# Kernel optimization log

Hardware: AMD Instinct MI355X
Metric: run time of the kernel (lower is better)

The kernel has to match this reference:

```python
import math
import jax, jax.numpy as jnp
import numpy as np

LN_EPS = 1e-5


def _layernorm(x, g, b):
    m = jnp.mean(x, axis=-1, keepdims=True)
    v = jnp.var(x, axis=-1, keepdims=True)
    return (x - m) / jnp.sqrt(v + LN_EPS) * g + b


def setup_inputs() -> dict:
    key = jax.random.key(0)
    ks = jax.random.split(key, 14)
    B, C, H, W = 8, 96, 224, 224
    dim, hidden = 96, int(96 * 4.0)

    def lin(k, i, o):
        return jax.random.normal(k, (i, o), jnp.float32) * 0.02

    return {
        "x": jax.random.normal(ks[0], (B, C, H, W), jnp.float32),
        "entropy_map": jax.random.uniform(ks[1], (B, 1, H, W), jnp.float32),
        "beta": jnp.float32(1.0),
        "wq": lin(ks[2], dim, dim), "bq": jnp.zeros((dim,), jnp.float32),
        "wk": lin(ks[3], dim, dim), "bk": jnp.zeros((dim,), jnp.float32),
        "wv": lin(ks[4], dim, dim), "bv": jnp.zeros((dim,), jnp.float32),
        "wo": lin(ks[5], dim, dim), "bo": jnp.zeros((dim,), jnp.float32),
        "ln1_g": jnp.ones((dim,), jnp.float32), "ln1_b": jnp.zeros((dim,), jnp.float32),
        "ln2_g": jnp.ones((dim,), jnp.float32), "ln2_b": jnp.zeros((dim,), jnp.float32),
        "w_fc1": lin(ks[6], dim, hidden), "b_fc1": jnp.zeros((hidden,), jnp.float32),
        "w_fc2": lin(ks[7], hidden, dim), "b_fc2": jnp.zeros((dim,), jnp.float32),
    }


def reference(x, entropy_map, beta, wq, bq, wk, bk, wv, bv, wo, bo,
              ln1_g, ln1_b, ln2_g, ln2_b, w_fc1, b_fc1, w_fc2, b_fc2):
    B, C, H, W = x.shape
    ws = 7
    num_heads = 4
    hd = C // num_heads
    nHw, nWw = H // ws, W // ws
    N = ws * ws

    # (B,C,H,W) -> (B,H,W,C), norm1
    xt = jnp.transpose(x, (0, 2, 3, 1))
    xn = _layernorm(xt, ln1_g, ln1_b)

    # window partition -> (B*nW, N, C)
    xw = xn.reshape(B, nHw, ws, nWw, ws, C).transpose(0, 1, 3, 2, 4, 5).reshape(-1, N, C)
    ew = entropy_map.transpose(0, 2, 3, 1).reshape(B, nHw, ws, nWw, ws, 1)
    ew = ew.transpose(0, 1, 3, 2, 4, 5).reshape(-1, N, 1)  # (Bw, N, 1)

    Bw = xw.shape[0]
    q = (jnp.einsum('bnc,cd->bnd', xw, wq) + bq).reshape(Bw, N, num_heads, hd).transpose(0, 2, 1, 3)
    k = (jnp.einsum('bnc,cd->bnd', xw, wk) + bk).reshape(Bw, N, num_heads, hd).transpose(0, 2, 1, 3)
    v = (jnp.einsum('bnc,cd->bnd', xw, wv) + bv).reshape(Bw, N, num_heads, hd).transpose(0, 2, 1, 3)

    scores = jnp.einsum('bhqd,bhkd->bhqk', q, k) / math.sqrt(hd)
    attn = jax.nn.softmax(scores, axis=-1)

    # entropy gating: per-query factor (Bw,1,N,1), then renormalize over keys
    gating = jnp.exp(-beta * ew)[:, None, :, :]
    attn = attn * gating
    attn = attn / (jnp.sum(attn, axis=-1, keepdims=True) + 1e-9)

    out = jnp.einsum('bhqk,bhkd->bhqd', attn, v).transpose(0, 2, 1, 3).reshape(Bw, N, C)
    out = jnp.einsum('bnc,cd->bnd', out, wo) + bo

    # window merge -> (B,H,W,C)
    out = out.reshape(B, nHw, nWw, ws, ws, C).transpose(0, 1, 3, 2, 4, 5).reshape(B, H, W, C)

    x_res = xt + out  # (B,H,W,C)

    # MLP branch
    xn2 = _layernorm(x_res, ln2_g, ln2_b)
    h = jax.nn.gelu(jnp.einsum('bhwc,cd->bhwd', xn2, w_fc1) + b_fc1, approximate=False)
    mlp_out = jnp.einsum('bhwd,dc->bhwc', h, w_fc2) + b_fc2

    x_out = x_res + mlp_out
    return jnp.transpose(x_out, (0, 3, 1, 2))  # (B,C,H,W)
```

## Files before the change

### kernel.cpp

```cpp
#include <hip/hip_runtime.h>
#include <math.h>

typedef __attribute__((ext_vector_type(8))) short short8;
typedef __attribute__((ext_vector_type(4))) float f32x4;
typedef __attribute__((ext_vector_type(4))) unsigned int uint4v;

struct __align__(8) U2 { unsigned int x, y; };

#define DEVI static __device__ __forceinline__

DEVI unsigned pk1(float f){ unsigned u = __float_as_uint(f); return (u + 0x7fffu + ((u>>16)&1u)) >> 16; }
DEVI unsigned pk2(float a, float b){ return pk1(a) | (pk1(b) << 16); }
DEVI float bfu(unsigned hs){ return __uint_as_float((hs & 0xffffu) << 16); }

DEVI short8 lds8(const unsigned short* p){
  union { short8 v; U2 u[2]; } f;
  f.u[0] = *(const U2*)p;
  f.u[1] = *(const U2*)(p + 4);
  return f.v;
}
DEVI short8 mk8(unsigned a, unsigned b, unsigned c, unsigned d){
  union { short8 v; unsigned u[4]; } f; f.u[0]=a; f.u[1]=b; f.u[2]=c; f.u[3]=d; return f.v;
}
DEVI short8 zero8(){ return mk8(0,0,0,0); }
DEVI short8 gfrag(const unsigned short* p){ union { short8 v; uint4v u; } f; f.u = *(const uint4v*)p; return f.v; }
DEVI f32x4 MFMA(short8 a, short8 b, f32x4 c){ return __builtin_amdgcn_mfma_f32_16x16x32_bf16(a, b, c, 0, 0, 0); }
DEVI void st2(unsigned short* p, unsigned lo, unsigned hi){ U2 t; t.x=lo; t.y=hi; *(U2*)p = t; }

DEVI float fastrcp(float x){ float r; asm("v_rcp_f32 %0, %1" : "=v"(r) : "v"(x)); return r; }
DEVI float gelu_f(float v){
  float z2 = fmaf(v*v*v, -0.07135481627f, -1.5957691216f*v);
  return v * fastrcp(1.f + __expf(z2));
}

__global__ __launch_bounds__(256) void prep_kernel(
    const float* __restrict__ wq, const float* __restrict__ wk,
    const float* __restrict__ wv, const float* __restrict__ wo,
    const float* __restrict__ w1, const float* __restrict__ w2,
    unsigned short* __restrict__ wfr)
{
  int i = blockIdx.x * 256 + threadIdx.x;
  if (i >= 110592) return;
  int j = i & 7, lane = (i >> 3) & 63, fr = i >> 9;
  int ln = lane & 15, lg = lane >> 4;
  float v;
  if (fr < 18)      { int s = fr;       int mt = s/3,  kb = s%3;  v = wq[(32*kb + 8*lg + j)*96  + 16*mt + ln]; }
  else if (fr < 36) { int s = fr - 18;  int mt = s/3,  kb = s%3;  v = wk[(32*kb + 8*lg + j)*96  + 16*mt + ln]; }
  else if (fr < 54) { int s = fr - 36;  int nt = s/3,  kb = s%3;  v = wv[(32*kb + 8*lg + j)*96  + 16*nt + ln]; }
  else if (fr < 72) { int s = fr - 54;  int mt = s/3,  kb = s%3;  v = wo[(32*kb + 8*lg + j)*96  + 16*mt + ln]; }
  else if (fr < 144){ int s = fr - 72;  int mt = s/3,  kb = s%3;  v = w1[(32*kb + 8*lg + j)*384 + 16*mt + ln]; }
  else              { int s = fr - 144; int mt = s/12, kb = s%12; v = w2[(32*kb + 8*lg + j)*96  + 16*mt + ln]; }
  wfr[i] = (unsigned short)pk1(v);
}

__global__ __launch_bounds__(256, 4) void attn_kernel(
    const float* __restrict__ x, const float* __restrict__ emap,
    const float* __restrict__ beta_p,
    const float* __restrict__ bq, const float* __restrict__ bk,
    const float* __restrict__ bv, const float* __restrict__ bo,
    const float* __restrict__ g1, const float* __restrict__ b1,
    const unsigned short* __restrict__ wfr,
    unsigned short* __restrict__ xres)
{
  __shared__ __align__(16) char smem[39744];
  unsigned short* XN = (unsigned short*)(smem);
  unsigned short* KS = (unsigned short*)(smem + 12800);
  unsigned short* VT = (unsigned short*)(smem + 25600);

  const int tid = threadIdx.x;
  const int lane = tid & 63;
  const int w = tid >> 6, lg = lane >> 4, ln = lane & 15;

  int bid = blockIdx.x;
  int bw  = ((bid & 7) << 10) | (bid >> 3);
  const int b  = bw >> 10;
  const int rr = bw & 1023;
  const int h0 = (rr >> 5) * 7;
  const int w0 = (rr & 31) * 7;

  for (int i = tid; i < 8*68; i += 256) VT[(96 + i/68)*68 + i%68] = 0;

  float ewv = 0.f;
  {
    const int t = 16*w + ln;
    float xv[24];
    if (t < 49){
      size_t pixloc = (size_t)(h0 + t/7)*224 + w0 + t%7;
      const float* xp = x + (size_t)(b*96 + 24*lg)*50176 + pixloc;
#pragma unroll
      for (int i = 0; i < 24; ++i) xv[i] = xp[(size_t)i*50176];
      ewv = emap[(size_t)b*50176 + pixloc];
    } else {
#pragma unroll
      for (int i = 0; i < 24; ++i) xv[i] = 0.f;
    }
    float s = 0.f, s2 = 0.f;
#pragma unroll
    for (int i = 0; i < 24; ++i){ s += xv[i]; s2 += xv[i]*xv[i]; }
    s  += __shfl_xor(s, 16);  s  += __shfl_xor(s, 32);
    s2 += __shfl_xor(s2, 16); s2 += __shfl_xor(s2, 32);
    float m = s * (1.f/96.f);
    float var = s2 * (1.f/96.f) - m*m;
    float rstd = rsqrtf(var + 1e-5f);
    unsigned* w32 = (unsigned*)(XN + t*100 + 24*lg);
    if (t < 49){
#pragma unroll
      for (int i = 0; i < 12; ++i){
        int c = 24*lg + 2*i;
        w32[i] = pk2((xv[2*i]   - m)*rstd*g1[c]   + b1[c],
                     (xv[2*i+1] - m)*rstd*g1[c+1] + b1[c+1]);
      }
    } else {
#pragma unroll
      for (int i = 0; i < 12; ++i) w32[i] = 0;
    }
  }
  __syncthreads();

  unsigned qp[6][2];
  {
    short8 bx0 = lds8(XN + (16*w+ln)*100 + 0  + 8*lg);
    short8 bx1 = lds8(XN + (16*w+ln)*100 + 32 + 8*lg);
    short8 bx2 = lds8(XN + (16*w+ln)*100 + 64 + 8*lg);
#pragma unroll
    for (int mt = 0; mt < 6; ++mt){
      int d0 = 16*mt + 4*lg;
      f32x4 aq, ak;
#pragma unroll
      for (int r = 0; r < 4; ++r){ aq[r] = bq[d0+r]; ak[r] = bk[d0+r]; }
      aq = MFMA(gfrag(wfr +        (mt*3+0)*512 + lane*8), bx0, aq);
      aq = MFMA(gfrag(wfr +        (mt*3+1)*512 + lane*8), bx1, aq);
      aq = MFMA(gfrag(wfr +        (mt*3+2)*512 + lane*8), bx2, aq);
      ak = MFMA(gfrag(wfr + 9216 + (mt*3+0)*512 + lane*8), bx0, ak);
      ak = MFMA(gfrag(wfr + 9216 + (mt*3+1)*512 + lane*8), bx1, ak);
      ak = MFMA(gfrag(wfr + 9216 + (mt*3+2)*512 + lane*8), bx2, ak);
      qp[mt][0] = pk2(aq[0],aq[1]);
      qp[mt][1] = pk2(aq[2],aq[3]);
      st2(KS + (16*w+ln)*100 + d0, pk2(ak[0],ak[1]), pk2(ak[2],ak[3]));
    }
#pragma unroll
    for (int f = 0; f < 6; ++f){
      int fl = f*4 + w;
      int mt = fl / 6, nt = fl % 6;
      float bvv = bv[16*nt + ln];
      f32x4 av; av[0]=bvv; av[1]=bvv; av[2]=bvv; av[3]=bvv;
#pragma unroll
      for (int kb = 0; kb < 3; ++kb)
        av = MFMA(lds8(XN + (16*mt+ln)*100 + 32*kb + 8*lg),
                  gfrag(wfr + 18432 + (nt*3+kb)*512 + lane*8), av);
      st2(VT + (16*nt+ln)*68 + 16*mt + 4*lg, pk2(av[0],av[1]), pk2(av[2],av[3]));
    }
  }
  __syncthreads();

  const float beta  = beta_p[0];
  const float scale = 0.20412414523193150818f;
  const float gq    = __expf(-beta * ewv);
  const int  psrcA  = ((lg & 1) << 5) + ln;
  const int  psrcB  = psrcA + 16;
  const bool phi    = (lg >= 2);

#pragma unroll
  for (int h = 0; h < 4; ++h){
    const int mlo = (6*h) >> 2, mhi = mlo + 1;
    const int thr = (h & 1) ? 1 : 2;
    int par  = (3*h + lg) & 1;
    int srcA = (par << 5) + ln;
    int srcB = srcA + 16;
    unsigned lA0 = __shfl(qp[mlo][0], srcA), lA1 = __shfl(qp[mlo][1], srcA);
    unsigned hA0 = __shfl(qp[mhi][0], srcA), hA1 = __shfl(qp[mhi][1], srcA);
    unsigned lB0 = __shfl(qp[mlo][0], srcB), lB1 = __shfl(qp[mlo][1], srcB);
    unsigned hB0 = __shfl(qp[mhi][0], srcB), hB1 = __shfl(qp[mhi][1], srcB);
    bool uh = (lg >= thr);
    short8 bqf = (lg < 3) ? mk8(uh?hA0:lA0, uh?hA1:lA1, uh?hB0:lB0, uh?hB1:lB1) : zero8();

    f32x4 sva[4];
#pragma unroll
    for (int mt = 0; mt < 4; ++mt){
      f32x4 z; z[0]=0.f; z[1]=0.f; z[2]=0.f; z[3]=0.f;
      short8 af = (lg < 3) ? lds8(KS + (16*mt+ln)*100 + 24*h + 8*lg) : zero8();
      sva[mt] = MFMA(af, bqf, z);
    }
    float vv[16]; float mx = -3e38f;
#pragma unroll
    for (int mt = 0; mt < 4; ++mt)
#pragma unroll
      for (int r = 0; r < 4; ++r){
        int key = 16*mt + 4*lg + r;
        float v = (key <= 48) ? sva[mt][r]*scale : -3e38f;
        vv[mt*4+r] = v; mx = fmaxf(mx, v);
      }
    mx = fmaxf(mx, __shfl_xor(mx, 16));
    mx = fmaxf(mx, __shfl_xor(mx, 32));
    float ssum = 0.f;
#pragma unroll
    for (int i = 0; i < 16; ++i){ float e = __expf(vv[i] - mx); vv[i] = e; ssum += e; }
    ssum += __shfl_xor(ssum, 16);
    ssum += __shfl_xor(ssum, 32);
    float inv = gq / (ssum * (gq + 1e-9f));

    unsigned pu[4][2];
#pragma unroll
    for (int mt = 0; mt < 4; ++mt){
      pu[mt][0] = pk2(vv[4*mt+0]*inv, vv[4*mt+1]*inv);
      pu[mt][1] = pk2(vv[4*mt+2]*inv, vv[4*mt+3]*inv);
    }
    unsigned a00=__shfl(pu[0][0],psrcA), a01=__shfl(pu[0][1],psrcA);
    unsigned a10=__shfl(pu[1][0],psrcA), a11=__shfl(pu[1][1],psrcA);
    unsigned b00=__shfl(pu[0][0],psrcB), b01=__shfl(pu[0][1],psrcB);
    unsigned b10=__shfl(pu[1][0],psrcB), b11=__shfl(pu[1][1],psrcB);
    short8 pf0 = mk8(phi?a10:a00, phi?a11:a01, phi?b10:b00, phi?b11:b01);
    unsigned c00=__shfl(pu[2][0],psrcA), c01=__shfl(pu[2][1],psrcA);
    unsigned c10=__shfl(pu[3][0],psrcA), c11=__shfl(pu[3][1],psrcA);
    unsigned d00=__shfl(pu[2][0],psrcB), d01=__shfl(pu[2][1],psrcB);
    unsigned d10=__shfl(pu[3][0],psrcB), d11=__shfl(pu[3][1],psrcB);
    short8 pf1 = mk8(phi?c10:c00, phi?c11:c01, phi?d10:d00, phi?d11:d01);

#pragma unroll
    for (int mt = 0; mt < 2; ++mt){
      f32x4 pv; pv[0]=0.f; pv[1]=0.f; pv[2]=0.f; pv[3]=0.f;
      pv = MFMA(lds8(VT + (24*h+16*mt+ln)*68 + 0  + 8*lg), pf0, pv);
      pv = MFMA(lds8(VT + (24*h+16*mt+ln)*68 + 32 + 8*lg), pf1, pv);
      if (!(mt == 1 && lg >= 2))
        st2(XN + (16*w+ln)*100 + 24*h + 16*mt + 4*lg, pk2(pv[0],pv[1]), pk2(pv[2],pv[3]));
    }
  }

  {
    f32x4 po[6];
#pragma unroll
    for (int mt = 0; mt < 6; ++mt){
      int c0 = 16*mt + 4*lg;
#pragma unroll
      for (int r = 0; r < 4; ++r) po[mt][r] = bo[c0+r];
    }
#pragma unroll
    for (int kb = 0; kb < 3; ++kb){
      short8 bf_ = lds8(XN + (16*w+ln)*100 + 32*kb + 8*lg);
#pragma unroll
      for (int mt = 0; mt < 6; ++mt)
        po[mt] = MFMA(gfrag(wfr + 27648 + (mt*3+kb)*512 + lane*8), bf_, po[mt]);
    }
    const int t = 16*w + ln;
    if (t < 49){
      size_t pixloc = (size_t)(h0 + t/7)*224 + w0 + t%7;
      const float* xp = x + (size_t)b*96*50176 + pixloc;
      unsigned short* xo = xres + ((size_t)b*50176 + pixloc)*96;
#pragma unroll
      for (int mt = 0; mt < 6; ++mt){
        int c0 = 16*mt + 4*lg;
        float r0 = po[mt][0] + xp[(size_t)(c0+0)*50176];
        float r1 = po[mt][1] + xp[(size_t)(c0+1)*50176];
        float r2 = po[mt][2] + xp[(size_t)(c0+2)*50176];
        float r3 = po[mt][3] + xp[(size_t)(c0+3)*50176];
        st2(xo + c0, pk2(r0,r1), pk2(r2,r3));
      }
    }
  }
}

__global__ __launch_bounds__(256, 4) void mlp_kernel(
    const unsigned short* __restrict__ xres,
    const float* __restrict__ g2, const float* __restrict__ b2,
    const float* __restrict__ bf1, const float* __restrict__ bf2,
    const unsigned short* __restrict__ wfr,
    float* __restrict__ out)
{
  __shared__ __align__(16) unsigned short XH[4][4800];
  const int tid = threadIdx.x, lane = tid & 63, w = tid >> 6;
  const int lg = lane >> 4, ln = lane & 15;
  unsigned short* XN2 = &XH[w][0];
  unsigned short* HS  = &XH[w][1600];

  const int tile = blockIdx.x*4 + w;
  const size_t p0 = (size_t)tile * 16;
  const int bimg = (int)(p0 / 50176);
  const size_t pixin = p0 - (size_t)bimg*50176;

  {
    const unsigned* xp = (const unsigned*)(xres + (p0 + (size_t)ln)*96 + 24*lg);
    float xv[24];
#pragma unroll
    for (int i = 0; i < 12; ++i){
      unsigned u = xp[i];
      xv[2*i] = bfu(u); xv[2*i+1] = bfu(u >> 16);
    }
    float s = 0.f, s2 = 0.f;
#pragma unroll
    for (int i = 0; i < 24; ++i){ s += xv[i]; s2 += xv[i]*xv[i]; }
    s  += __shfl_xor(s, 16);  s  += __shfl_xor(s, 32);
    s2 += __shfl_xor(s2, 16); s2 += __shfl_xor(s2, 32);
    float m = s * (1.f/96.f);
    float var = s2 * (1.f/96.f) - m*m;
    float rstd = rsqrtf(var + 1e-5f);
    unsigned* w32 = (unsigned*)(XN2 + ln*100 + 24*lg);
#pragma unroll
    for (int i = 0; i < 12; ++i){
      int c = 24*lg + 2*i;
      w32[i] = pk2((xv[2*i]   - m)*rstd*g2[c]   + b2[c],
                   (xv[2*i+1] - m)*rstd*g2[c+1] + b2[c+1]);
    }
  }

  f32x4 oacc[6];
#pragma unroll
  for (int mt = 0; mt < 6; ++mt){
    int c0 = 16*mt + 4*lg;
#pragma unroll
    for (int r = 0; r < 4; ++r) oacc[mt][r] = bf2[c0+r];
  }

  short8 bxx0 = lds8(XN2 + ln*100 + 0  + 8*lg);
  short8 bxx1 = lds8(XN2 + ln*100 + 32 + 8*lg);
  short8 bxx2 = lds8(XN2 + ln*100 + 64 + 8*lg);

#pragma unroll
  for (int p = 0; p < 2; ++p){
#pragma unroll
    for (int mt = 0; mt < 12; ++mt){
      int hg = p*192 + 16*mt + 4*lg;
      f32x4 ha;
#pragma unroll
      for (int r = 0; r < 4; ++r) ha[r] = bf1[hg+r];
      ha = MFMA(gfrag(wfr + 36864 + ((p*12+mt)*3+0)*512 + lane*8), bxx0, ha);
      ha = MFMA(gfrag(wfr + 36864 + ((p*12+mt)*3+1)*512 + lane*8), bxx1, ha);
      ha = MFMA(gfrag(wfr + 36864 + ((p*12+mt)*3+2)*512 + lane*8), bxx2, ha);
      st2(HS + ln*200 + 16*mt + 4*lg,
          pk2(gelu_f(ha[0]), gelu_f(ha[1])), pk2(gelu_f(ha[2]), gelu_f(ha[3])));
    }
#pragma unroll
    for (int kb = 0; kb < 6; ++kb){
      short8 bh = lds8(HS + ln*200 + 32*kb + 8*lg);
#pragma unroll
      for (int mt = 0; mt < 6; ++mt)
        oacc[mt] = MFMA(gfrag(wfr + 73728 + (mt*12 + p*6 + kb)*512 + lane*8), bh, oacc[mt]);
    }
  }

  {
    const unsigned short* xr = xres + (p0 + (size_t)ln)*96;
    float* ob = out + (size_t)bimg*96*50176 + pixin + ln;
#pragma unroll
    for (int mt = 0; mt < 6; ++mt){
      int c0 = 16*mt + 4*lg;
      U2 rv = *(const U2*)(xr + c0);
      ob[(size_t)(c0+0)*50176] = oacc[mt][0] + bfu(rv.x);
      ob[(size_t)(c0+1)*50176] = oacc[mt][1] + bfu(rv.x >> 16);
      ob[(size_t)(c0+2)*50176] = oacc[mt][2] + bfu(rv.y);
      ob[(size_t)(c0+3)*50176] = oacc[mt][3] + bfu(rv.y >> 16);
    }
  }
}

extern "C" void kernel_launch(void* const* d_in, const int* in_sizes, int n_in,
                              void* d_out, int out_size, void* d_ws, size_t ws_size,
                              hipStream_t stream) {
  const float* x    = (const float*)d_in[0];
  const float* emap = (const float*)d_in[1];
  const float* beta = (const float*)d_in[2];
  const float* wq   = (const float*)d_in[3];
  const float* bq   = (const float*)d_in[4];
  const float* wk   = (const float*)d_in[5];
  const float* bk   = (const float*)d_in[6];
  const float* wv   = (const float*)d_in[7];
  const float* bv   = (const float*)d_in[8];
  const float* wo   = (const float*)d_in[9];
  const float* bo   = (const float*)d_in[10];
  const float* g1   = (const float*)d_in[11];
  const float* b1   = (const float*)d_in[12];
  const float* g2   = (const float*)d_in[13];
  const float* b2   = (const float*)d_in[14];
  const float* w1   = (const float*)d_in[15];
  const float* bf1  = (const float*)d_in[16];
  const float* w2   = (const float*)d_in[17];
  const float* bf2  = (const float*)d_in[18];

  float* out = (float*)d_out;
  unsigned short* wfr  = (unsigned short*)d_ws;
  unsigned short* xres = (unsigned short*)((char*)d_ws + 262144);

  prep_kernel<<<dim3(432), dim3(256), 0, stream>>>(wq, wk, wv, wo, w1, w2, wfr);
  attn_kernel<<<dim3(8192), dim3(256), 0, stream>>>(
      x, emap, beta, bq, bk, bv, bo, g1, b1, wfr, xres);
  mlp_kernel<<<dim3(6272), dim3(256), 0, stream>>>(
      xres, g2, b2, bf1, bf2, wfr, out);
}
```

Before: 429.9 us.

## Fold attention scale into Wq, drop softmax max, reuse loaded x for residuals

Pre-scales Wq and bq by 1/sqrt(hd) so scores need no extra multiply. The softmax max-reduction is replaced by a fixed -50 bias on padded keys, and normalization moves to the P·V output via a fast reciprocal. Q is now staged through LDS instead of register shuffles. The x values loaded for LayerNorm are kept in registers and reused for the residual add in both kernels, removing a second global read of x and of xres. This uses more LDS and registers, so occupancy drops from 4 to 3 blocks. Dropping the max subtraction assumes scores stay small enough for exp not to overflow.

```diff
diff --git a/kernel.cpp b/kernel.cpp
--- a/kernel.cpp
+++ b/kernel.cpp
@@ -44,7 +44,7 @@
   int j = i & 7, lane = (i >> 3) & 63, fr = i >> 9;
   int ln = lane & 15, lg = lane >> 4;
   float v;
-  if (fr < 18)      { int s = fr;       int mt = s/3,  kb = s%3;  v = wq[(32*kb + 8*lg + j)*96  + 16*mt + ln]; }
+  if (fr < 18)      { int s = fr;       int mt = s/3,  kb = s%3;  v = wq[(32*kb + 8*lg + j)*96  + 16*mt + ln] * 0.20412414523193150818f; }
   else if (fr < 36) { int s = fr - 18;  int mt = s/3,  kb = s%3;  v = wk[(32*kb + 8*lg + j)*96  + 16*mt + ln]; }
   else if (fr < 54) { int s = fr - 36;  int nt = s/3,  kb = s%3;  v = wv[(32*kb + 8*lg + j)*96  + 16*nt + ln]; }
   else if (fr < 72) { int s = fr - 54;  int mt = s/3,  kb = s%3;  v = wo[(32*kb + 8*lg + j)*96  + 16*mt + ln]; }
@@ -53,7 +53,7 @@
   wfr[i] = (unsigned short)pk1(v);
 }
 
-__global__ __launch_bounds__(256, 4) void attn_kernel(
+__global__ __launch_bounds__(256, 3) void attn_kernel(
     const float* __restrict__ x, const float* __restrict__ emap,
     const float* __restrict__ beta_p,
     const float* __restrict__ bq, const float* __restrict__ bk,
@@ -62,10 +62,11 @@
     const unsigned short* __restrict__ wfr,
     unsigned short* __restrict__ xres)
 {
-  __shared__ __align__(16) char smem[39744];
+  __shared__ __align__(16) char smem[52544];
   unsigned short* XN = (unsigned short*)(smem);
-  unsigned short* KS = (unsigned short*)(smem + 12800);
-  unsigned short* VT = (unsigned short*)(smem + 25600);
+  unsigned short* QS = (unsigned short*)(smem + 12800);
+  unsigned short* KS = (unsigned short*)(smem + 25600);
+  unsigned short* VT = (unsigned short*)(smem + 38400);
 
   const int tid = threadIdx.x;
   const int lane = tid & 63;
@@ -78,17 +79,18 @@
   const int h0 = (rr >> 5) * 7;
   const int w0 = (rr & 31) * 7;
 
-  for (int i = tid; i < 8*68; i += 256) VT[(96 + i/68)*68 + i%68] = 0;
-
+  const int t = 16*w + ln;
+
+  float xv[24];
   float ewv = 0.f;
   {
-    const int t = 16*w + ln;
-    float xv[24];
     if (t < 49){
       size_t pixloc = (size_t)(h0 + t/7)*224 + w0 + t%7;
-      const float* xp = x + (size_t)(b*96 + 24*lg)*50176 + pixloc;
-#pragma unroll
-      for (int i = 0; i < 24; ++i) xv[i] = xp[(size_t)i*50176];
+      const float* xp = x + (size_t)(b*96 + 4*lg)*50176 + pixloc;
+#pragma unroll
+      for (int mt = 0; mt < 6; ++mt)
+#pragma unroll
+        for (int r = 0; r < 4; ++r) xv[mt*4+r] = xp[(size_t)(16*mt + r)*50176];
       ewv = emap[(size_t)b*50176 + pixloc];
     } else {
 #pragma unroll
@@ -102,41 +104,40 @@
     float m = s * (1.f/96.f);
     float var = s2 * (1.f/96.f) - m*m;
     float rstd = rsqrtf(var + 1e-5f);
-    unsigned* w32 = (unsigned*)(XN + t*100 + 24*lg);
+    unsigned short* row = XN + t*100;
     if (t < 49){
 #pragma unroll
-      for (int i = 0; i < 12; ++i){
-        int c = 24*lg + 2*i;
-        w32[i] = pk2((xv[2*i]   - m)*rstd*g1[c]   + b1[c],
-                     (xv[2*i+1] - m)*rstd*g1[c+1] + b1[c+1]);
+      for (int mt = 0; mt < 6; ++mt){
+        int c0 = 16*mt + 4*lg;
+        st2(row + c0,
+            pk2((xv[4*mt+0]-m)*rstd*g1[c0+0]+b1[c0+0], (xv[4*mt+1]-m)*rstd*g1[c0+1]+b1[c0+1]),
+            pk2((xv[4*mt+2]-m)*rstd*g1[c0+2]+b1[c0+2], (xv[4*mt+3]-m)*rstd*g1[c0+3]+b1[c0+3]));
       }
     } else {
 #pragma unroll
-      for (int i = 0; i < 12; ++i) w32[i] = 0;
+      for (int mt = 0; mt < 6; ++mt) st2(row + 16*mt + 4*lg, 0u, 0u);
     }
   }
   __syncthreads();
 
-  unsigned qp[6][2];
-  {
-    short8 bx0 = lds8(XN + (16*w+ln)*100 + 0  + 8*lg);
-    short8 bx1 = lds8(XN + (16*w+ln)*100 + 32 + 8*lg);
-    short8 bx2 = lds8(XN + (16*w+ln)*100 + 64 + 8*lg);
+  {
+    short8 bx0 = lds8(XN + t*100 + 0  + 8*lg);
+    short8 bx1 = lds8(XN + t*100 + 32 + 8*lg);
+    short8 bx2 = lds8(XN + t*100 + 64 + 8*lg);
 #pragma unroll
     for (int mt = 0; mt < 6; ++mt){
       int d0 = 16*mt + 4*lg;
       f32x4 aq, ak;
 #pragma unroll
-      for (int r = 0; r < 4; ++r){ aq[r] = bq[d0+r]; ak[r] = bk[d0+r]; }
+      for (int r = 0; r < 4; ++r){ aq[r] = bq[d0+r]*0.20412414523193150818f; ak[r] = bk[d0+r]; }
       aq = MFMA(gfrag(wfr +        (mt*3+0)*512 + lane*8), bx0, aq);
       aq = MFMA(gfrag(wfr +        (mt*3+1)*512 + lane*8), bx1, aq);
       aq = MFMA(gfrag(wfr +        (mt*3+2)*512 + lane*8), bx2, aq);
       ak = MFMA(gfrag(wfr + 9216 + (mt*3+0)*512 + lane*8), bx0, ak);
       ak = MFMA(gfrag(wfr + 9216 + (mt*3+1)*512 + lane*8), bx1, ak);
       ak = MFMA(gfrag(wfr + 9216 + (mt*3+2)*512 + lane*8), bx2, ak);
-      qp[mt][0] = pk2(aq[0],aq[1]);
-      qp[mt][1] = pk2(aq[2],aq[3]);
-      st2(KS + (16*w+ln)*100 + d0, pk2(ak[0],ak[1]), pk2(ak[2],ak[3]));
+      st2(QS + t*100 + d0, pk2(aq[0],aq[1]), pk2(aq[2],aq[3]));
+      st2(KS + t*100 + d0, pk2(ak[0],ak[1]), pk2(ak[2],ak[3]));
     }
 #pragma unroll
     for (int f = 0; f < 6; ++f){
@@ -153,57 +154,39 @@
   }
   __syncthreads();
 
-  const float beta  = beta_p[0];
-  const float scale = 0.20412414523193150818f;
-  const float gq    = __expf(-beta * ewv);
-  const int  psrcA  = ((lg & 1) << 5) + ln;
-  const int  psrcB  = psrcA + 16;
-  const bool phi    = (lg >= 2);
+  const float beta = beta_p[0];
+  const float gq   = __expf(-beta * ewv);
+  const float gfac = gq / (gq + 1e-9f);
+  const int  psrcA = ((lg & 1) << 5) + ln;
+  const int  psrcB = psrcA + 16;
+  const bool phi   = (lg >= 2);
+
+  f32x4 mz;  mz[0]=0.f; mz[1]=0.f; mz[2]=0.f; mz[3]=0.f;
+  f32x4 m3;
+#pragma unroll
+  for (int r = 0; r < 4; ++r) m3[r] = (4*lg + r >= 1) ? -50.f : 0.f;
 
 #pragma unroll
   for (int h = 0; h < 4; ++h){
-    const int mlo = (6*h) >> 2, mhi = mlo + 1;
-    const int thr = (h & 1) ? 1 : 2;
-    int par  = (3*h + lg) & 1;
-    int srcA = (par << 5) + ln;
-    int srcB = srcA + 16;
-    unsigned lA0 = __shfl(qp[mlo][0], srcA), lA1 = __shfl(qp[mlo][1], srcA);
-    unsigned hA0 = __shfl(qp[mhi][0], srcA), hA1 = __shfl(qp[mhi][1], srcA);
-    unsigned lB0 = __shfl(qp[mlo][0], srcB), lB1 = __shfl(qp[mlo][1], srcB);
-    unsigned hB0 = __shfl(qp[mhi][0], srcB), hB1 = __shfl(qp[mhi][1], srcB);
-    bool uh = (lg >= thr);
-    short8 bqf = (lg < 3) ? mk8(uh?hA0:lA0, uh?hA1:lA1, uh?hB0:lB0, uh?hB1:lB1) : zero8();
-
+    short8 bqf = (lg < 3) ? lds8(QS + t*100 + 24*h + 8*lg) : zero8();
     f32x4 sva[4];
 #pragma unroll
     for (int mt = 0; mt < 4; ++mt){
-      f32x4 z; z[0]=0.f; z[1]=0.f; z[2]=0.f; z[3]=0.f;
       short8 af = (lg < 3) ? lds8(KS + (16*mt+ln)*100 + 24*h + 8*lg) : zero8();
-      sva[mt] = MFMA(af, bqf, z);
-    }
-    float vv[16]; float mx = -3e38f;
-#pragma unroll
-    for (int mt = 0; mt < 4; ++mt)
-#pragma unroll
-      for (int r = 0; r < 4; ++r){
-        int key = 16*mt + 4*lg + r;
-        float v = (key <= 48) ? sva[mt][r]*scale : -3e38f;
-        vv[mt*4+r] = v; mx = fmaxf(mx, v);
-      }
-    mx = fmaxf(mx, __shfl_xor(mx, 16));
-    mx = fmaxf(mx, __shfl_xor(mx, 32));
-    float ssum = 0.f;
-#pragma unroll
-    for (int i = 0; i < 16; ++i){ float e = __expf(vv[i] - mx); vv[i] = e; ssum += e; }
+      sva[mt] = MFMA(af, bqf, (mt == 3) ? m3 : mz);
+    }
+    float vv[16]; float ssum = 0.f;
+#pragma unroll
+    for (int i = 0; i < 16; ++i){ float e = __expf(sva[i>>2][i&3]); vv[i] = e; ssum += e; }
     ssum += __shfl_xor(ssum, 16);
     ssum += __shfl_xor(ssum, 32);
-    float inv = gq / (ssum * (gq + 1e-9f));
+    float inv = gfac * fastrcp(ssum);
 
     unsigned pu[4][2];
 #pragma unroll
     for (int mt = 0; mt < 4; ++mt){
-      pu[mt][0] = pk2(vv[4*mt+0]*inv, vv[4*mt+1]*inv);
-      pu[mt][1] = pk2(vv[4*mt+2]*inv, vv[4*mt+3]*inv);
+      pu[mt][0] = pk2(vv[4*mt+0], vv[4*mt+1]);
+      pu[mt][1] = pk2(vv[4*mt+2], vv[4*mt+3]);
     }
     unsigned a00=__shfl(pu[0][0],psrcA), a01=__shfl(pu[0][1],psrcA);
     unsigned a10=__shfl(pu[1][0],psrcA), a11=__shfl(pu[1][1],psrcA);
@@ -222,7 +205,8 @@
       pv = MFMA(lds8(VT + (24*h+16*mt+ln)*68 + 0  + 8*lg), pf0, pv);
       pv = MFMA(lds8(VT + (24*h+16*mt+ln)*68 + 32 + 8*lg), pf1, pv);
       if (!(mt == 1 && lg >= 2))
-        st2(XN + (16*w+ln)*100 + 24*h + 16*mt + 4*lg, pk2(pv[0],pv[1]), pk2(pv[2],pv[3]));
+        st2(XN + t*100 + 24*h + 16*mt + 4*lg,
+            pk2(pv[0]*inv, pv[1]*inv), pk2(pv[2]*inv, pv[3]*inv));
     }
   }
 
@@ -236,24 +220,20 @@
     }
 #pragma unroll
     for (int kb = 0; kb < 3; ++kb){
-      short8 bf_ = lds8(XN + (16*w+ln)*100 + 32*kb + 8*lg);
+      short8 bf_ = lds8(XN + t*100 + 32*kb + 8*lg);
 #pragma unroll
       for (int mt = 0; mt < 6; ++mt)
         po[mt] = MFMA(gfrag(wfr + 27648 + (mt*3+kb)*512 + lane*8), bf_, po[mt]);
     }
-    const int t = 16*w + ln;
     if (t < 49){
       size_t pixloc = (size_t)(h0 + t/7)*224 + w0 + t%7;
-      const float* xp = x + (size_t)b*96*50176 + pixloc;
       unsigned short* xo = xres + ((size_t)b*50176 + pixloc)*96;
 #pragma unroll
       for (int mt = 0; mt < 6; ++mt){
         int c0 = 16*mt + 4*lg;
-        float r0 = po[mt][0] + xp[(size_t)(c0+0)*50176];
-        float r1 = po[mt][1] + xp[(size_t)(c0+1)*50176];
-        float r2 = po[mt][2] + xp[(size_t)(c0+2)*50176];
-        float r3 = po[mt][3] + xp[(size_t)(c0+3)*50176];
-        st2(xo + c0, pk2(r0,r1), pk2(r2,r3));
+        st2(xo + c0,
+            pk2(po[mt][0] + xv[4*mt+0], po[mt][1] + xv[4*mt+1]),
+            pk2(po[mt][2] + xv[4*mt+2], po[mt][3] + xv[4*mt+3]));
       }
     }
   }
@@ -277,13 +257,14 @@
   const int bimg = (int)(p0 / 50176);
   const size_t pixin = p0 - (size_t)bimg*50176;
 
-  {
-    const unsigned* xp = (const unsigned*)(xres + (p0 + (size_t)ln)*96 + 24*lg);
-    float xv[24];
-#pragma unroll
-    for (int i = 0; i < 12; ++i){
-      unsigned u = xp[i];
-      xv[2*i] = bfu(u); xv[2*i+1] = bfu(u >> 16);
+  float xv[24];
+  {
+    const unsigned short* xp = xres + (p0 + (size_t)ln)*96;
+#pragma unroll
+    for (int mt = 0; mt < 6; ++mt){
+      U2 u = *(const U2*)(xp + 16*mt + 4*lg);
+      xv[4*mt+0] = bfu(u.x); xv[4*mt+1] = bfu(u.x >> 16);
+      xv[4*mt+2] = bfu(u.y); xv[4*mt+3] = bfu(u.y >> 16);
     }
     float s = 0.f, s2 = 0.f;
 #pragma unroll
@@ -293,12 +274,12 @@
     float m = s * (1.f/96.f);
     float var = s2 * (1.f/96.f) - m*m;
     float rstd = rsqrtf(var + 1e-5f);
-    unsigned* w32 = (unsigned*)(XN2 + ln*100 + 24*lg);
-#pragma unroll
-    for (int i = 0; i < 12; ++i){
-      int c = 24*lg + 2*i;
-      w32[i] = pk2((xv[2*i]   - m)*rstd*g2[c]   + b2[c],
-                   (xv[2*i+1] - m)*rstd*g2[c+1] + b2[c+1]);
+#pragma unroll
+    for (int mt = 0; mt < 6; ++mt){
+      int c0 = 16*mt + 4*lg;
+      st2(XN2 + ln*100 + c0,
+          pk2((xv[4*mt+0]-m)*rstd*g2[c0+0]+b2[c0+0], (xv[4*mt+1]-m)*rstd*g2[c0+1]+b2[c0+1]),
+          pk2((xv[4*mt+2]-m)*rstd*g2[c0+2]+b2[c0+2], (xv[4*mt+3]-m)*rstd*g2[c0+3]+b2[c0+3]));
     }
   }
 
@@ -338,16 +319,14 @@
   }
 
   {
-    const unsigned short* xr = xres + (p0 + (size_t)ln)*96;
     float* ob = out + (size_t)bimg*96*50176 + pixin + ln;
 #pragma unroll
     for (int mt = 0; mt < 6; ++mt){
       int c0 = 16*mt + 4*lg;
-      U2 rv = *(const U2*)(xr + c0);
-      ob[(size_t)(c0+0)*50176] = oacc[mt][0] + bfu(rv.x);
-      ob[(size_t)(c0+1)*50176] = oacc[mt][1] + bfu(rv.x >> 16);
-      ob[(size_t)(c0+2)*50176] = oacc[mt][2] + bfu(rv.y);
-      ob[(size_t)(c0+3)*50176] = oacc[mt][3] + bfu(rv.y >> 16);
+      ob[(size_t)(c0+0)*50176] = oacc[mt][0] + xv[4*mt+0];
+      ob[(size_t)(c0+1)*50176] = oacc[mt][1] + xv[4*mt+1];
+      ob[(size_t)(c0+2)*50176] = oacc[mt][2] + xv[4*mt+2];
+      ob[(size_t)(c0+3)*50176] = oacc[mt][3] + xv[4*mt+3];
     }
   }
 }
```

Measured after the change: 507.9 us. +18.2%, slower.
